# Performance work log

Hardware: AMD Instinct MI355X
Metric: run time of the kernel (lower is better)

The kernel has to match this reference:

```python
import jax, jax.numpy as jnp
import numpy as np

CONF_T = 0.01
IOU_T = 0.45
NNS_K = 300     # max detections per class
K_TOTAL = 200   # max total detections
B, N, C = 16, 8732, 20  # batch, anchors, classes (feature dim = 1 + C + 4)


def setup_inputs() -> dict:
    key = jax.random.key(0)
    k1, k2 = jax.random.split(key, 2)
    # columns [0] background-ish score (ignored), [1:1+C] class scores, [-4:] boxes
    scores = jax.random.uniform(k1, (B, N, 1 + C), dtype=jnp.float32)
    # build valid [y1, x1, y2, x2] boxes in [0,1] from two random corner points
    pts = jax.random.uniform(k2, (B, N, 2, 2), dtype=jnp.float32)
    lo = jnp.min(pts, axis=2)   # [B,N,2] -> (y1,x1)
    hi = jnp.max(pts, axis=2)   # [B,N,2] -> (y2,x2)
    boxes = jnp.concatenate([lo, hi], axis=-1)
    inputs = jnp.concatenate([scores, boxes], axis=-1)  # [B,N,25]
    return {"inputs": inputs}


def _iou_one_vs_many(box, boxes):
    # box: [4] (y1,x1,y2,x2); boxes: [K,4]
    y1 = jnp.maximum(box[0], boxes[:, 0])
    x1 = jnp.maximum(box[1], boxes[:, 1])
    y2 = jnp.minimum(box[2], boxes[:, 2])
    x2 = jnp.minimum(box[3], boxes[:, 3])
    inter = jnp.maximum(y2 - y1, 0.0) * jnp.maximum(x2 - x1, 0.0)
    a = (box[2] - box[0]) * (box[3] - box[1])
    b = (boxes[:, 2] - boxes[:, 0]) * (boxes[:, 3] - boxes[:, 1])
    union = a + b - inter
    return jnp.where(union > 0.0, inter / union, 0.0)


def _nms_single_class(scores, boxes):
    # scores: [N], boxes: [N,4]. Greedy NMS over score-sorted candidates,
    # keeping up to NNS_K boxes in a fixed-size selection buffer.
    order = jnp.argsort(-scores)
    s = scores[order]
    b = boxes[order]

    def step(carry, xs):
        sel_b, sel_s, cnt = carry
        box, sc = xs
        occupied = sel_s > 0.0  # selected slots (scores > CONF_T > 0)
        iou = _iou_one_vs_many(box, sel_b)
        suppressed = jnp.any((iou > IOU_T) & occupied)
        keep = (sc > CONF_T) & jnp.logical_not(suppressed) & (cnt < NNS_K)
        idx = jnp.minimum(cnt, NNS_K - 1)
        sel_b = sel_b.at[idx].set(jnp.where(keep, box, sel_b[idx]))
        sel_s = sel_s.at[idx].set(jnp.where(keep, sc, sel_s[idx]))
        cnt = cnt + keep.astype(jnp.int32)
        return (sel_b, sel_s, cnt), None

    init = (jnp.zeros((NNS_K, 4), s.dtype),
            jnp.full((NNS_K,), -1.0, s.dtype),
            jnp.int32(0))
    (sel_b, sel_s, _), _ = jax.lax.scan(step, init, (b, s))
    return sel_s, sel_b


def reference(inputs) -> jnp.ndarray:
    boxes = inputs[..., -4:]                 # [B,N,4], shared across classes (q=1)
    cls_scores = inputs[:, :, 1:-4]          # [B,N,C]
    sc = jnp.transpose(cls_scores, (0, 2, 1))  # [B,C,N]

    # per-class NMS, vmapped over class (boxes shared) then batch
    nms = jax.vmap(jax.vmap(_nms_single_class, in_axes=(0, None)), in_axes=(0, 0))
    sel_s, sel_b = nms(sc, boxes)            # [B,C,NNS_K], [B,C,NNS_K,4]

    cls_ids = jnp.broadcast_to(
        jnp.arange(C, dtype=inputs.dtype)[None, :, None], (B, C, NNS_K))

    flat_s = sel_s.reshape(B, C * NNS_K)
    flat_b = sel_b.reshape(B, C * NNS_K, 4)
    flat_c = cls_ids.reshape(B, C * NNS_K)

    # combine across classes: global top-k by score (padding slots have score -1)
    top_s, top_i = jax.lax.top_k(flat_s, K_TOTAL)          # [B,K_TOTAL]
    top_b = jnp.take_along_axis(flat_b, top_i[..., None], axis=1)
    top_c = jnp.take_along_axis(flat_c, top_i, axis=1)

    valid = top_s > 0.0
    scores_o = jnp.where(valid, top_s, 0.0)
    boxes_o = jnp.where(valid[..., None], jnp.clip(top_b, 0.0, 1.0), 0.0)  # clip_boxes=True default
    classes_o = jnp.where(valid, top_c, 0.0) + 1.0  # layer adds 1 (padding -> class 1, as in TF)

    return jnp.concatenate(
        [classes_o[..., None], scores_o[..., None], boxes_o], axis=-1)  # [B,K_TOTAL,6]
```

## Files before the change

### kernel.cpp

```cpp
#include <hip/hip_runtime.h>

typedef unsigned long long u64;
typedef unsigned int u32;

namespace {
constexpr int kB = 16;
constexpr int kN = 8732;
constexpr int kC = 20;
constexpr int kRow = 25;
constexpr int kKeep = 300;
constexpr int kSel = 200;
constexpr int kTot = 200;
constexpr float kConf = 0.01f;
constexpr double kThr = 0.45000000298023223876953125;

constexpr int TPB = 512;
constexpr int NW = TPB / 64;
constexpr int NBKT = 4096;
constexpr int kPool = 512;
constexpr int kFlat = kC * kKeep;
constexpr int kNIter = (kN + TPB - 1) / TPB;
}

__device__ __forceinline__ bool iou_gt4(const float4 a, const float aa,
                                        const float4 b, const float ba) {
  const float ty1 = fmaxf(a.x, b.x);
  const float tx1 = fmaxf(a.y, b.y);
  const float ty2 = fminf(a.z, b.z);
  const float tx2 = fminf(a.w, b.w);
  const float dy = fmaxf(__fsub_rn(ty2, ty1), 0.0f);
  const float dx = fmaxf(__fsub_rn(tx2, tx1), 0.0f);
  const float inter = __fmul_rn(dy, dx);
  const float uni = __fsub_rn(__fadd_rn(aa, ba), inter);
  return ((double)inter > kThr * (double)uni);
}

__device__ __forceinline__ int bkt_of(float s) {
  return 65024 - (int)(__float_as_uint(s) >> 14);
}
__device__ __forceinline__ u32 key_of(float s, int idx) {
  return ((__float_as_uint(s) & 0x3FFFu) << 14) | (u32)(16383 - idx);
}
__device__ __forceinline__ u64 mkey(float s, u32 f) {
  return (s > 0.0f) ? ((((u64)__float_as_uint(s)) << 32) | (u64)(0xFFFFFFFFu - f))
                    : 0ull;
}

__device__ int excl_scan_hist(u32* hist, u32* wsum, int tid) {
  const int base = tid * 8;
  u32 loc[8];
  u32 s = 0;
#pragma unroll
  for (int i = 0; i < 8; ++i) { loc[i] = hist[base + i]; s += loc[i]; }
  int v = (int)s;
  const int lane = tid & 63;
#pragma unroll
  for (int off = 1; off < 64; off <<= 1) {
    const int u = __shfl_up(v, off);
    if (lane >= off) v += u;
  }
  if (lane == 63) wsum[tid >> 6] = (u32)v;
  __syncthreads();
  u32 woff = 0, total = 0;
#pragma unroll
  for (int w = 0; w < NW; ++w) {
    const u32 t = wsum[w];
    total += t;
    if (w < (tid >> 6)) woff += t;
  }
  u32 run = woff + (u32)v - s;
#pragma unroll
  for (int i = 0; i < 8; ++i) { hist[base + i] = run; run += loc[i]; }
  __syncthreads();
  return (int)total;
}

__global__ __launch_bounds__(256) void prep_kernel(const float* __restrict__ in,
                                                   float* __restrict__ st,
                                                   float4* __restrict__ pbox) {
  const int b = blockIdx.y;
  const int n0 = blockIdx.x * 256;
  const int tid = threadIdx.x;
  const int rows = min(256, kN - n0);

  __shared__ float tile[256 * kRow];
  const float* __restrict__ src = in + ((size_t)b * kN + n0) * kRow;
  const int total = rows * kRow;
  for (int i = tid; i < total; i += 256) tile[i] = src[i];
  __syncthreads();
  if (tid < rows) {
    const int n = n0 + tid;
    const float* row = &tile[tid * kRow];
#pragma unroll
    for (int c = 0; c < kC; ++c)
      st[((size_t)b * kC + c) * kN + n] = row[1 + c];
    pbox[(size_t)b * kN + n] = make_float4(row[21], row[22], row[23], row[24]);
  }
}

template <bool X>
__global__ __launch_bounds__(TPB, 4) void nms_kernel(const float* __restrict__ in,
                                                     const float* __restrict__ st,
                                                     const float4* __restrict__ pbox,
                                                     float* __restrict__ ws_s,
                                                     float* __restrict__ ws_b) {
  const int task = blockIdx.x;
  const int b = task / kC;
  const int c = task - b * kC;
  const int tid = threadIdx.x;
  const float* __restrict__ base_in = in + (size_t)b * kN * kRow;
  const float* __restrict__ stc = st + ((size_t)b * kC + c) * kN;
  const size_t bo = (size_t)b * kN;

  __shared__ __align__(16) unsigned char ovl[16384];
  __shared__ u32 skey[kPool];
  __shared__ float4 sel_box[kSel];
  __shared__ float sel_ar[kSel];
  __shared__ float sel_sc[kSel];
  __shared__ u32 supp8[NW * 64];
  __shared__ u64 grp8[NW * 64];
  __shared__ u32 wsum[NW];
  __shared__ int s_red[NW];
  __shared__ int s_nc;

  u32* hist = (u32*)ovl;
  float4* gbox = (float4*)ovl;
  float* gar = (float*)(ovl + 8192);
  float* gsc = (float*)(ovl + 10240);

  const int lane = tid & 63;
  const int wid = tid >> 6;

  int cnt = 0;
  int blo = 0;
  while (cnt < kSel && blo < NBKT) {
    for (int i = tid; i < NBKT; i += TPB) hist[i] = 0;
    __syncthreads();
    for (int k = 0; k < kNIter; ++k) {
      const int n = tid + k * TPB;
      if (n < kN) {
        const float s = X ? stc[n] : base_in[(size_t)n * kRow + 1 + c];
        if (s > kConf) atomicAdd(&hist[bkt_of(s)], 1u);
      }
    }
    __syncthreads();
    const int ncand = excl_scan_hist(hist, wsum, tid);
    const int base = (int)hist[blo];
    if (ncand == 0 || base >= ncand) break;
    int bestb = blo + 1;
#pragma unroll
    for (int i = 0; i < 8; ++i) {
      const int bb = tid * 8 + i;
      if (bb > blo && (int)hist[bb] - base <= kPool) bestb = max(bestb, bb);
    }
    if (ncand - base <= kPool) bestb = NBKT;
#pragma unroll
    for (int off = 32; off; off >>= 1) bestb = max(bestb, __shfl_xor(bestb, off));
    if (lane == 0) s_red[wid] = bestb;
    __syncthreads();
    int bend = s_red[0];
#pragma unroll
    for (int w = 1; w < NW; ++w) bend = max(bend, s_red[w]);
    const int poolN =
        min(((bend == NBKT) ? ncand : (int)hist[bend]) - base, kPool);
    for (int k = 0; k < kNIter; ++k) {
      const int n = tid + k * TPB;
      if (n < kN) {
        const float s = X ? stc[n] : base_in[(size_t)n * kRow + 1 + c];
        if (s > kConf) {
          const int bb = bkt_of(s);
          if (bb >= blo && bb < bend) {
            const u32 pos = atomicAdd(&hist[bb], 1u) - (u32)base;
            if (pos < (u32)kPool) skey[pos] = key_of(s, n);
          }
        }
      }
    }
    __syncthreads();
    for (int bb = blo + tid; bb < bend; bb += TPB) {
      int s0 = (bb == blo) ? 0 : (int)hist[bb - 1] - base;
      int e0 = (int)hist[bb] - base;
      s0 = min(s0, kPool);
      e0 = min(e0, kPool);
      for (int i = s0 + 1; i < e0; ++i) {
        const u32 kk = skey[i];
        int j = i - 1;
        while (j >= s0 && kk > skey[j]) { skey[j + 1] = skey[j]; --j; }
        skey[j + 1] = kk;
      }
    }
    __syncthreads();
    for (int i = tid; i < poolN; i += TPB) {
      const int eidx = 16383 - (int)(skey[i] & 0x3FFFu);
      float4 bx;
      float s;
      if (X) {
        bx = pbox[bo + eidx];
        s = stc[eidx];
      } else {
        const float* r = base_in + (size_t)eidx * kRow;
        bx = make_float4(r[21], r[22], r[23], r[24]);
        s = r[1 + c];
      }
      gbox[i] = bx;
      gar[i] = __fmul_rn(__fsub_rn(bx.z, bx.x), __fsub_rn(bx.w, bx.y));
      gsc[i] = s;
    }
    __syncthreads();

    int g0 = 0;
    while (cnt < kSel && g0 < poolN) {
      const int i = g0 + lane;
      u32 sup = 1u;
      u64 rowbits = 0;
      if (i < poolN) {
        sup = 0u;
        const float4 eb = gbox[i];
        const float ea = gar[i];
        for (int j = wid; j < cnt; j += NW)
          sup |= iou_gt4(eb, ea, sel_box[j], sel_ar[j]) ? 1u : 0u;
        for (int t2 = wid; t2 < lane; t2 += NW)
          rowbits |= iou_gt4(eb, ea, gbox[g0 + t2], gar[g0 + t2])
                         ? (1ull << t2)
                         : 0ull;
      }
      supp8[wid * 64 + lane] = sup;
      grp8[wid * 64 + lane] = rowbits;
      __syncthreads();
      if (tid < 64) {
        u32 sp = 0;
        u64 row = 0;
#pragma unroll
        for (int s2 = 0; s2 < NW; ++s2) {
          sp |= supp8[s2 * 64 + tid];
          row |= grp8[s2 * 64 + tid];
        }
        const u64 pend = __ballot(sp == 0u);
        u64 acc = 0;
        int nc = cnt;
        if (cnt + __popcll(pend) <= kSel) {
          const u64 consb = __ballot(row != 0ull);
          acc = pend & ~consb;
          u64 rem = pend & consb;
          while (rem != 0ull) {
            const int cur = __ffsll(rem) - 1;
            const u64 cb = 1ull << cur;
            const u64 rcur = __shfl(row, cur);
            if ((rcur & acc) == 0ull) acc |= cb;
            rem &= ~cb;
          }
          nc = cnt + (int)__popcll(acc);
        } else {
          u64 pend2 = pend;
          while (pend2 != 0ull && nc < kSel) {
            const int cur = __ffsll(pend2) - 1;
            const u64 cb = 1ull << cur;
            acc |= cb;
            ++nc;
            const u64 killed = __ballot(((row >> cur) & 1ull) != 0ull);
            pend2 &= ~(killed | cb);
          }
        }
        if ((acc >> tid) & 1ull) {
          const int slot = cnt + (int)__popcll(acc & ((1ull << tid) - 1ull));
          const int ii = g0 + tid;
          sel_box[slot] = gbox[ii];
          sel_ar[slot] = gar[ii];
          sel_sc[slot] = gsc[ii];
        }
        if (tid == 0) s_nc = nc;
      }
      __syncthreads();
      cnt = s_nc;
      g0 += 64;
    }
    blo = bend;
  }

  float* __restrict__ out_s = ws_s + (size_t)task * kKeep;
  float* __restrict__ out_b = ws_b + (size_t)task * kKeep * 4;
  for (int i = tid; i < kKeep; i += TPB) {
    if (i < cnt) {
      out_s[i] = sel_sc[i];
      *(float4*)&out_b[(size_t)i * 4] = sel_box[i];
    } else {
      out_s[i] = -1.0f;
    }
  }
}

__global__ __launch_bounds__(256) void topk_kernel(const float* __restrict__ ws_s,
                                                   const float* __restrict__ ws_b,
                                                   float* __restrict__ out) {
  const int task = blockIdx.x;
  const int b = task / kC;
  const int c = task - b * kC;
  const int tid = threadIdx.x;
  const int lane = tid & 63;
  const float* __restrict__ ss = ws_s + (size_t)b * kFlat;
  const float4* __restrict__ bb4 = (const float4*)ws_b + (size_t)b * kFlat;
  float* __restrict__ ob = out + (size_t)b * kTot * 6;

  __shared__ u64 key[kC * kTot];
  __shared__ int rnk[kTot];
  __shared__ int s_v;

  for (int p = tid; p < kC * kTot; p += 256) {
    const int cc = p / kTot;
    const int i = p - cc * kTot;
    const u32 f = (u32)(cc * kKeep + i);
    key[p] = mkey(ss[f], f);
  }
  for (int i = tid; i < kTot; i += 256) rnk[i] = i;
  if (tid == 0) s_v = 0;
  __syncthreads();

  int myv = 0;
  for (int p = tid; p < kC * kTot; p += 256) myv += (key[p] != 0ull) ? 1 : 0;
#pragma unroll
  for (int off = 32; off; off >>= 1) myv += __shfl_xor(myv, off);
  if (lane == 0) atomicAdd(&s_v, myv);

  const u64* __restrict__ myk = &key[c * kTot];
  for (int t = tid; t < kTot * (kC - 1); t += 256) {
    const int i = t / (kC - 1);
    int c2 = t - i * (kC - 1);
    c2 += (c2 >= c) ? 1 : 0;
    const u64 k = myk[i];
    if (k == 0ull) continue;
    const u64* __restrict__ seg = &key[c2 * kTot];
    int lo = 0, hi = kTot;
    while (lo < hi) {
      const int mid = (lo + hi) >> 1;
      if (seg[mid] > k) lo = mid + 1;
      else hi = mid;
    }
    if (lo) atomicAdd(&rnk[i], lo);
  }
  __syncthreads();

  for (int i = tid; i < kTot; i += 256) {
    const u64 k = myk[i];
    if (k == 0ull) continue;
    const int r = rnk[i];
    if (r < kTot) {
      const u32 f = 0xFFFFFFFFu - (u32)(k & 0xFFFFFFFFull);
      const float4 bx = bb4[f];
      ob[r * 6 + 0] = (float)(c + 1);
      ob[r * 6 + 1] = __uint_as_float((u32)(k >> 32));
      ob[r * 6 + 2] = fminf(fmaxf(bx.x, 0.0f), 1.0f);
      ob[r * 6 + 3] = fminf(fmaxf(bx.y, 0.0f), 1.0f);
      ob[r * 6 + 4] = fminf(fmaxf(bx.z, 0.0f), 1.0f);
      ob[r * 6 + 5] = fminf(fmaxf(bx.w, 0.0f), 1.0f);
    }
  }
  if (c == 0) {
    const int v0 = min(s_v, kTot);
    for (int r = v0 + tid; r < kTot; r += 256) {
      ob[r * 6 + 0] = 1.0f;
      ob[r * 6 + 1] = 0.0f;
      ob[r * 6 + 2] = 0.0f;
      ob[r * 6 + 3] = 0.0f;
      ob[r * 6 + 4] = 0.0f;
      ob[r * 6 + 5] = 0.0f;
    }
  }
}

extern "C" void kernel_launch(void* const* d_in, const int* in_sizes, int n_in,
                              void* d_out, int out_size, void* d_ws, size_t ws_size,
                              hipStream_t stream) {
  const float* in = (const float*)d_in[0];
  float* out = (float*)d_out;
  float* ws_s = (float*)d_ws;
  float* ws_b = ws_s + (size_t)kB * kC * kKeep;
  float* st = ws_b + (size_t)kB * kC * kKeep * 4;
  float4* pbox = (float4*)(st + (size_t)kB * kC * kN);
  const size_t needed =
      ((size_t)kB * kC * kKeep * 5 + (size_t)kB * kC * kN + (size_t)kB * kN * 4) *
      sizeof(float);
  if (ws_size >= needed) {
    prep_kernel<<<dim3((kN + 255) / 256, kB), dim3(256), 0, stream>>>(in, st,
                                                                      pbox);
    nms_kernel<true><<<dim3(kB * kC), dim3(TPB), 0, stream>>>(in, st, pbox,
                                                              ws_s, ws_b);
  } else {
    nms_kernel<false><<<dim3(kB * kC), dim3(TPB), 0, stream>>>(
        in, nullptr, nullptr, ws_s, ws_b);
  }
  topk_kernel<<<dim3(kB * kC), dim3(256), 0, stream>>>(ws_s, ws_b, out);
}
```

Baseline: 88.63 us.

## Track per-candidate suppression incrementally against newly accepted boxes in NMS

Each thread now owns one pool candidate and tests it once against the boxes already selected when the pool is built. After each 64-candidate group is resolved, it only tests against the boxes accepted in that group, and keeps a per-wave alive mask in shared memory. The old code recomputed IoU for every group against the whole growing selection list. The aim is to cut redundant IoU work, at the cost of a serial per-thread loop over prior selections and an extra ballot and shared-memory bookkeeping per group.

Measured after the change: 118.0 us. 33.1% more time.

```diff
diff --git a/kernel.cpp b/kernel.cpp
--- a/kernel.cpp
+++ b/kernel.cpp
@@ -117,11 +117,13 @@
   __shared__ float4 sel_box[kSel];
   __shared__ float sel_ar[kSel];
   __shared__ float sel_sc[kSel];
-  __shared__ u32 supp8[NW * 64];
-  __shared__ u64 grp8[NW * 64];
+  __shared__ u64 rows8[NW][64];
+  __shared__ int alist[64];
+  __shared__ u64 aliveW[NW];
   __shared__ u32 wsum[NW];
   __shared__ int s_red[NW];
   __shared__ int s_nc;
+  __shared__ int s_nacc;
 
   u32* hist = (u32*)ovl;
   float4* gbox = (float4*)ovl;
@@ -208,34 +210,41 @@
     }
     __syncthreads();
 
-    int g0 = 0;
-    while (cnt < kSel && g0 < poolN) {
-      const int i = g0 + lane;
-      u32 sup = 1u;
-      u64 rowbits = 0;
-      if (i < poolN) {
-        sup = 0u;
-        const float4 eb = gbox[i];
-        const float ea = gar[i];
-        for (int j = wid; j < cnt; j += NW)
-          sup |= iou_gt4(eb, ea, sel_box[j], sel_ar[j]) ? 1u : 0u;
-        for (int t2 = wid; t2 < lane; t2 += NW)
-          rowbits |= iou_gt4(eb, ea, gbox[g0 + t2], gar[g0 + t2])
-                         ? (1ull << t2)
-                         : 0ull;
-      }
-      supp8[wid * 64 + lane] = sup;
-      grp8[wid * 64 + lane] = rowbits;
+    float4 myb = make_float4(0, 0, 0, 0);
+    float mya = 0.0f;
+    u32 mysup = 1u;
+    if (tid < poolN) {
+      myb = gbox[tid];
+      mya = gar[tid];
+      mysup = 0u;
+      for (int j = 0; j < cnt; ++j)
+        mysup |= iou_gt4(myb, mya, sel_box[j], sel_ar[j]) ? 1u : 0u;
+    }
+    {
+      const u64 wb = __ballot(mysup == 0u);
+      if (lane == 0) aliveW[wid] = wb;
+    }
+    int g = 0;
+    while (cnt < kSel && g * 64 < poolN) {
+      const int g0 = g * 64;
+      {
+        const int i = g0 + lane;
+        u64 rb = 0;
+        if (i < poolN) {
+          const float4 eb = gbox[i];
+          const float ea = gar[i];
+          for (int t2 = wid; t2 < lane; t2 += NW)
+            rb |= iou_gt4(eb, ea, gbox[g0 + t2], gar[g0 + t2]) ? (1ull << t2)
+                                                               : 0ull;
+        }
+        rows8[wid][lane] = rb;
+      }
       __syncthreads();
       if (tid < 64) {
-        u32 sp = 0;
-        u64 row = 0;
-#pragma unroll
-        for (int s2 = 0; s2 < NW; ++s2) {
-          sp |= supp8[s2 * 64 + tid];
-          row |= grp8[s2 * 64 + tid];
-        }
-        const u64 pend = __ballot(sp == 0u);
+        u64 row = rows8[0][tid];
+#pragma unroll
+        for (int s2 = 1; s2 < NW; ++s2) row |= rows8[s2][tid];
+        const u64 pend = aliveW[g];
         u64 acc = 0;
         int nc = cnt;
         if (cnt + __popcll(pend) <= kSel) {
@@ -262,17 +271,35 @@
           }
         }
         if ((acc >> tid) & 1ull) {
-          const int slot = cnt + (int)__popcll(acc & ((1ull << tid) - 1ull));
+          const int ord = (int)__popcll(acc & ((1ull << tid) - 1ull));
+          const int slot = cnt + ord;
           const int ii = g0 + tid;
           sel_box[slot] = gbox[ii];
           sel_ar[slot] = gar[ii];
           sel_sc[slot] = gsc[ii];
-        }
-        if (tid == 0) s_nc = nc;
+          alist[ord] = ii;
+        }
+        if (tid == 0) {
+          s_nc = nc;
+          s_nacc = (int)__popcll(acc);
+        }
       }
       __syncthreads();
+      const int nacc = s_nacc;
+      if (mysup == 0u) {
+        u32 hit = 0u;
+        for (int j = 0; j < nacc; ++j) {
+          const int a = alist[j];
+          hit |= (a != tid && iou_gt4(myb, mya, gbox[a], gar[a])) ? 1u : 0u;
+        }
+        mysup |= hit;
+      }
+      {
+        const u64 wb = __ballot(mysup == 0u);
+        if (lane == 0) aliveW[wid] = wb;
+      }
       cnt = s_nc;
-      g0 += 64;
+      ++g;
     }
     blo = bend;
   }
```
